# Performance work log

Hardware: AMD Instinct MI355X
Metric: run time of the kernel (lower is better)

## Reference

```python
import jax, jax.numpy as jnp
import numpy as np

B, C, H, W, K = 2, 36, 512, 512, 9
GROUPS, GSIZE = 3, 12  # channel groups 0:12, 12:24, 24:36


def _grid_sample_bilinear(feat, gx, gy):
    """Bilinear grid_sample, align_corners=True. feat [B,C,H,W]; gx,gy [B,H,W] in [-1,1]."""
    Bn, Cn, Hn, Wn = feat.shape
    px = (gx + 1.0) * 0.5 * (Wn - 1)
    py = (gy + 1.0) * 0.5 * (Hn - 1)
    x0 = jnp.floor(px)
    y0 = jnp.floor(py)
    wx = (px - x0)[:, None, :, :]
    wy = (py - y0)[:, None, :, :]
    x0i = jnp.clip(x0.astype(jnp.int32), 0, Wn - 1)
    x1i = jnp.clip(x0i + 1, 0, Wn - 1)
    y0i = jnp.clip(y0.astype(jnp.int32), 0, Hn - 1)
    y1i = jnpip = jnp.clip(y0.astype(jnp.int32) + 1, 0, Hn - 1)
    flat = feat.reshape(Bn, Cn, Hn * Wn)
    gather = jax.vmap(lambda f, yi, xi: f[:, yi * Wn + xi])  # -> [B,C,H,W]
    v00 = gather(flat, y0i, x0i)
    v01 = gather(flat, y0i, x1i)
    v10 = gather(flat, y1i, x0i)
    v11 = gather(flat, y1i, x1i)
    return (v00 * (1 - wx) * (1 - wy) + v01 * wx * (1 - wy)
            + v10 * (1 - wx) * wy + v11 * wx * wy)


def setup_inputs() -> dict:
    key = jax.random.key(0)
    k1, k2, k3 = jax.random.split(key, 3)
    features = jax.random.normal(k1, (B, C, H, W), jnp.float32)
    offset_x = jax.random.normal(k2, (B, K, H, W), jnp.float32) * 16.0
    offset_y = jax.random.normal(k3, (B, K, H, W), jnp.float32) * 16.0
    left_x = jnp.broadcast_to(jnp.arange(W, dtype=jnp.float32)[None, None, None, :], (B, 1, H, W))
    left_y = jnp.broadcast_to(jnp.arange(H, dtype=jnp.float32)[None, None, :, None], (B, 1, H, W))
    return {"features": features, "offset_x": offset_x, "offset_y": offset_y,
            "left_x": jnp.array(left_x), "left_y": jnp.array(left_y)}


def reference(features, offset_x, offset_y, left_x, left_y):
    Hn, Wn = features.shape[2], features.shape[3]
    # clamp candidate coords to image, then normalize to [-1,1]
    rx = jnp.clip(left_x + offset_x, 0.0, Wn - 1)
    ry = jnp.clip(left_y + offset_y, 0.0, Hn - 1)
    gx = (rx - (Wn - 1) / 2.0) / ((Wn - 1) / 2.0)  # [B,K,H,W]
    gy = (ry - (Hn - 1) / 2.0) / ((Hn - 1) / 2.0)

    def per_candidate(g):
        gxk, gyk = g  # each [B,H,W]
        a = _grid_sample_bilinear(features, gxk, gyk)  # [B,36,H,W]
        a2 = jnp.roll(a, 12, axis=1)
        a3 = jnp.roll(a, 24, axis=1)

        def grp_mean(d):  # [B,36,H,W] -> [B,3,H,W] mean over 12-channel groups
            return d.reshape(d.shape[0], GROUPS, GSIZE, d.shape[2], d.shape[3]).mean(axis=2)

        s = jnp.concatenate([grp_mean(-jnp.abs(features - a)),
                             grp_mean(-jnp.abs(features - a2)),
                             grp_mean(-jnp.abs(features - a3))], axis=1)  # [B,9,H,W]
        return jnp.max(s, axis=1)  # top-1 of sort == max  -> [B,H,W]

    strengths = jax.lax.map(per_candidate,
                            (jnp.moveaxis(gx, 1, 0), jnp.moveaxis(gy, 1, 0)))  # [K,B,H,W]
    strengths = jnp.moveaxis(strengths, 0, 1)  # [B,K,H,W]

    wgt = jax.nn.softmax(strengths * 1000.0, axis=1)
    ox = jnp.sum(offset_x * wgt, axis=1, keepdims=True)
    oy = jnp.sum(offset_y * wgt, axis=1, keepdims=True)
    oy = jnp.clip(oy + left_y, 0.0, Hn - 1) - left_y
    ox = jnp.clip(ox + left_x, 0.0, Wn - 1) - left_x
    return ox, oy
```

## Files before the change

kernel.cpp:

```cpp
#include <hip/hip_runtime.h>
#include <math.h>

#define B_ 2
#define C_ 36
#define H_ 512
#define W_ 512
#define K_ 9
#define HW_ (H_ * W_)
#define ROWF4 (W_ * C_ / 4)

__global__ __launch_bounds__(256) void transpose_kernel(const float* __restrict__ in,
                                                        float* __restrict__ out) {
  __shared__ float tile[64][37];
  int blk = blockIdx.x;
  int wt = blk & 7;
  int h = (blk >> 3) & (H_ - 1);
  int b = blk >> 12;
  int w0 = wt << 6;
  int tid = threadIdx.x;
  const float* src = in + ((size_t)b * C_) * HW_ + (size_t)h * W_ + w0;
#pragma unroll
  for (int it = 0; it < 9; ++it) {
    int idx = it * 256 + tid;
    int c = idx >> 6;
    int wl = idx & 63;
    tile[wl][c] = src[(size_t)c * HW_ + wl];
  }
  __syncthreads();
  float* dst = out + (((size_t)b * H_ + h) * W_ + w0) * C_;
#pragma unroll
  for (int it = 0; it < 9; ++it) {
    int idx = it * 256 + tid;
    int wl = idx / 36;
    int c = idx - wl * 36;
    dst[idx] = tile[wl][c];
  }
}

__global__ __launch_bounds__(64) void eval_kernel_cw(const float* __restrict__ feat,
                                                     const float* __restrict__ offx,
                                                     const float* __restrict__ offy,
                                                     float* __restrict__ out) {
  __shared__ __align__(16) float F_lds[64 * 36];
  __shared__ __align__(16) float4 w_lds[64];
  __shared__ int a_lds[64];
  __shared__ float xk_lds[64 * 9];

  int tid = threadIdx.x;
  int blk = blockIdx.x;
  int region = blk & 7;
  int slot = blk >> 3;
  int b = region >> 2;
  int qd = region & 3;
  int qy = (qd >> 1) << 8;
  int qx = (qd & 1) << 8;
  int tr = slot >> 5;
  int tc = slot & 31;
  if (tr & 1) tc = 31 - tc;
  int h = qy + tr * 8 + (tid >> 3);
  int w = qx + tc * 8 + (tid & 7);
  int ph = h * W_ + w;
  int p = b * HW_ + ph;

  const float4* feat4 = reinterpret_cast<const float4*>(feat);

  {
    const float4* myF = feat4 + (size_t)p * 9;
#pragma unroll
    for (int i = 0; i < 9; ++i) {
      float4 v = myF[i];
      *reinterpret_cast<float4*>(&F_lds[tid * 36 + 4 * i]) = v;
    }
  }

  int g = tid / 9;
  int q = tid - 9 * g;
  int qm3 = q % 3;
  int fofs = 4 * qm3;

  float lx = (float)w;
  float ly = (float)h;
  const float* oxb = offx + (size_t)b * K_ * HW_ + ph;
  const float* oyb = offy + (size_t)b * K_ * HW_ + ph;

  __syncthreads();

#pragma unroll 1
  for (int k = 0; k < K_; ++k) {
    float ox = oxb[k * HW_];
    float oy = oyb[k * HW_];
    float rx = fminf(fmaxf(lx + ox, 0.0f), 511.0f);
    float ry = fminf(fmaxf(ly + oy, 0.0f), 511.0f);
    float gx = (rx - 255.5f) / 255.5f;
    float gy = (ry - 255.5f) / 255.5f;
    float px = (gx + 1.0f) * 0.5f * 511.0f;
    float py = (gy + 1.0f) * 0.5f * 511.0f;
    int x0 = (int)floorf(px); x0 = (x0 > 510) ? 510 : x0;
    int y0 = (int)floorf(py); y0 = (y0 > 510) ? 510 : y0;
    float wx = px - (float)x0;
    float wy = py - (float)y0;
    float4 wv = make_float4((1.0f - wx) * (1.0f - wy), wx * (1.0f - wy),
                            (1.0f - wx) * wy, wx * wy);
    w_lds[tid] = wv;
    a_lds[tid] = ((b * H_ + y0) * W_ + x0) * 9;
    __syncthreads();

    for (int r = 0; r < 10; ++r) {
      int tt = 7 * r + g;
      int t = (tt > 63) ? 63 : tt;
      int tb = a_lds[t];
      float4 W4 = w_lds[t];
      const float4* r0 = feat4 + tb;
      float4 v00 = r0[q];
      float4 v01 = r0[9 + q];
      float4 v10 = r0[ROWF4 + q];
      float4 v11 = r0[ROWF4 + 9 + q];
      float4 a4;
      a4.x = W4.x * v00.x + W4.y * v01.x + W4.z * v10.x + W4.w * v11.x;
      a4.y = W4.x * v00.y + W4.y * v01.y + W4.z * v10.y + W4.w * v11.y;
      a4.z = W4.x * v00.z + W4.y * v01.z + W4.z * v10.z + W4.w * v11.z;
      a4.w = W4.x * v00.w + W4.y * v01.w + W4.z * v10.w + W4.w * v11.w;
      const float* fl = &F_lds[t * 36 + fofs];
      float4 f0 = *reinterpret_cast<const float4*>(fl);
      float4 f1 = *reinterpret_cast<const float4*>(fl + 12);
      float4 f2 = *reinterpret_cast<const float4*>(fl + 24);
      float pf0 = fabsf(f0.x - a4.x) + fabsf(f0.y - a4.y) +
                  fabsf(f0.z - a4.z) + fabsf(f0.w - a4.w);
      float pf1 = fabsf(f1.x - a4.x) + fabsf(f1.y - a4.y) +
                  fabsf(f1.z - a4.z) + fabsf(f1.w - a4.w);
      float pf2 = fabsf(f2.x - a4.x) + fabsf(f2.y - a4.y) +
                  fabsf(f2.z - a4.z) + fabsf(f2.w - a4.w);
      float d0 = pf0 + __shfl(pf0, tid + 1) + __shfl(pf0, tid + 2);
      float d1 = pf1 + __shfl(pf1, tid + 1) + __shfl(pf1, tid + 2);
      float d2 = pf2 + __shfl(pf2, tid + 1) + __shfl(pf2, tid + 2);
      float mn3 = fminf(d0, fminf(d1, d2));
      float mn = fminf(mn3, fminf(__shfl(mn3, tid + 3), __shfl(mn3, tid + 6)));
      if (q == 0 && g < 7 && tt < 64) {
        xk_lds[tt * 9 + k] = -(mn / 12.0f) * 1000.0f;
      }
    }
    __syncthreads();
  }

  float M = -INFINITY;
#pragma unroll
  for (int k = 0; k < K_; ++k) M = fmaxf(M, xk_lds[tid * 9 + k]);
  float den = 0.f, ax = 0.f, ay = 0.f;
#pragma unroll
  for (int k = 0; k < K_; ++k) {
    float e = expf(xk_lds[tid * 9 + k] - M);
    den += e;
    ax += e * oxb[k * HW_];
    ay += e * oyb[k * HW_];
  }
  float resx = ax / den;
  float resy = ay / den;
  out[p] = fminf(fmaxf(resx + lx, 0.0f), 511.0f) - lx;
  out[B_ * HW_ + p] = fminf(fmaxf(resy + ly, 0.0f), 511.0f) - ly;
}

__global__ __launch_bounds__(256) void eval_kernel_n(const float* __restrict__ feat,
                                                     const float* __restrict__ offx,
                                                     const float* __restrict__ offy,
                                                     float* __restrict__ out) {
  int p = blockIdx.x * 256 + threadIdx.x;
  int ph = p & (HW_ - 1);
  int b = p >> 18;
  float F[C_];
  const float* fb = feat + (size_t)b * C_ * HW_ + ph;
#pragma unroll
  for (int c = 0; c < C_; ++c) F[c] = fb[(size_t)c * HW_];
  float lx = (float)(ph & (W_ - 1));
  float ly = (float)((ph >> 9) & (H_ - 1));
  const float* oxb = offx + (size_t)b * K_ * HW_ + ph;
  const float* oyb = offy + (size_t)b * K_ * HW_ + ph;
  float M = -INFINITY, den = 0.f, ax = 0.f, ay = 0.f;
#pragma unroll 1
  for (int k = 0; k < K_; ++k) {
    float ox = oxb[k * HW_];
    float oy = oyb[k * HW_];
    float rx = fminf(fmaxf(lx + ox, 0.0f), 511.0f);
    float ry = fminf(fmaxf(ly + oy, 0.0f), 511.0f);
    float gx = (rx - 255.5f) / 255.5f;
    float gy = (ry - 255.5f) / 255.5f;
    float px = (gx + 1.0f) * 0.5f * 511.0f;
    float py = (gy + 1.0f) * 0.5f * 511.0f;
    int x0 = (int)floorf(px); x0 = (x0 > 510) ? 510 : x0;
    int y0 = (int)floorf(py); y0 = (y0 > 510) ? 510 : y0;
    float wx = px - (float)x0;
    float wy = py - (float)y0;
    float w00 = (1.0f - wx) * (1.0f - wy);
    float w01 = wx * (1.0f - wy);
    float w10 = (1.0f - wx) * wy;
    float w11 = wx * wy;
    float D[9] = {0.f, 0.f, 0.f, 0.f, 0.f, 0.f, 0.f, 0.f, 0.f};
    const float* pl = feat + (size_t)b * C_ * HW_ + (size_t)y0 * W_ + x0;
#pragma unroll
    for (int c = 0; c < C_; ++c) {
      const float* q0 = pl + (size_t)c * HW_;
      float v00 = q0[0], v01 = q0[1];
      float v10 = q0[W_], v11 = q0[W_ + 1];
      float a = v00 * w00 + v01 * w01 + v10 * w10 + v11 * w11;
      int i = c % 12;
      int ga = c / 12;
      D[ga]     += fabsf(F[i]      - a);
      D[3 + ga] += fabsf(F[12 + i] - a);
      D[6 + ga] += fabsf(F[24 + i] - a);
    }
    float mn = D[0];
#pragma unroll
    for (int j = 1; j < 9; ++j) mn = fminf(mn, D[j]);
    float xk = -(mn / 12.0f) * 1000.0f;
    float nm = fmaxf(M, xk);
    float sc = expf(M - nm);
    float ek = expf(xk - nm);
    den = den * sc + ek;
    ax = ax * sc + ox * ek;
    ay = ay * sc + oy * ek;
    M = nm;
  }
  float resx = ax / den;
  float resy = ay / den;
  out[p] = fminf(fmaxf(resx + lx, 0.0f), 511.0f) - lx;
  out[B_ * HW_ + p] = fminf(fmaxf(resy + ly, 0.0f), 511.0f) - ly;
}

extern "C" void kernel_launch(void* const* d_in, const int* in_sizes, int n_in,
                              void* d_out, int out_size, void* d_ws, size_t ws_size,
                              hipStream_t stream) {
  const float* features = (const float*)d_in[0];
  const float* offset_x = (const float*)d_in[1];
  const float* offset_y = (const float*)d_in[2];
  float* out = (float*)d_out;

  const int npix = B_ * HW_;
  const size_t need = (size_t)npix * C_ * sizeof(float);

  if (ws_size >= need) {
    float* featT = (float*)d_ws;
    transpose_kernel<<<B_ * H_ * (W_ / 64), 256, 0, stream>>>(features, featT);
    eval_kernel_cw<<<npix / 64, 64, 0, stream>>>(featT, offset_x, offset_y, out);
  } else {
    eval_kernel_n<<<npix / 256, 256, 0, stream>>>(features, offset_x, offset_y, out);
  }
}
```

Baseline: 349.1 us.

## Split bilinear gather from per-pixel distance reduction via LDS scratch

```diff
diff --git a/kernel.cpp b/kernel.cpp
--- a/kernel.cpp
+++ b/kernel.cpp
@@ -37,14 +37,13 @@
   }
 }
 
-__global__ __launch_bounds__(64) void eval_kernel_cw(const float* __restrict__ feat,
-                                                     const float* __restrict__ offx,
-                                                     const float* __restrict__ offy,
-                                                     float* __restrict__ out) {
-  __shared__ __align__(16) float F_lds[64 * 36];
+__global__ __launch_bounds__(64, 4) void eval_kernel_cw(const float* __restrict__ feat,
+                                                        const float* __restrict__ offx,
+                                                        const float* __restrict__ offy,
+                                                        float* __restrict__ out) {
+  __shared__ __align__(16) float scratch[64 * 36];
   __shared__ __align__(16) float4 w_lds[64];
   __shared__ int a_lds[64];
-  __shared__ float xk_lds[64 * 9];
 
   int tid = threadIdx.x;
   int blk = blockIdx.x;
@@ -64,26 +63,25 @@
 
   const float4* feat4 = reinterpret_cast<const float4*>(feat);
 
+  float F[C_];
   {
     const float4* myF = feat4 + (size_t)p * 9;
 #pragma unroll
     for (int i = 0; i < 9; ++i) {
       float4 v = myF[i];
-      *reinterpret_cast<float4*>(&F_lds[tid * 36 + 4 * i]) = v;
+      F[4 * i + 0] = v.x; F[4 * i + 1] = v.y; F[4 * i + 2] = v.z; F[4 * i + 3] = v.w;
     }
   }
 
   int g = tid / 9;
   int q = tid - 9 * g;
-  int qm3 = q % 3;
-  int fofs = 4 * qm3;
 
   float lx = (float)w;
   float ly = (float)h;
   const float* oxb = offx + (size_t)b * K_ * HW_ + ph;
   const float* oyb = offy + (size_t)b * K_ * HW_ + ph;
 
-  __syncthreads();
+  float M = -INFINITY, den = 0.f, axs = 0.f, ays = 0.f;
 
 #pragma unroll 1
   for (int k = 0; k < K_; ++k) {
@@ -99,14 +97,14 @@
     int y0 = (int)floorf(py); y0 = (y0 > 510) ? 510 : y0;
     float wx = px - (float)x0;
     float wy = py - (float)y0;
-    float4 wv = make_float4((1.0f - wx) * (1.0f - wy), wx * (1.0f - wy),
-                            (1.0f - wx) * wy, wx * wy);
-    w_lds[tid] = wv;
+    w_lds[tid] = make_float4((1.0f - wx) * (1.0f - wy), wx * (1.0f - wy),
+                             (1.0f - wx) * wy, wx * wy);
     a_lds[tid] = ((b * H_ + y0) * W_ + x0) * 9;
     __syncthreads();
 
+    int tt = g;
+#pragma unroll 1
     for (int r = 0; r < 10; ++r) {
-      int tt = 7 * r + g;
       int t = (tt > 63) ? 63 : tt;
       int tb = a_lds[t];
       float4 W4 = w_lds[t];
@@ -120,41 +118,44 @@
       a4.y = W4.x * v00.y + W4.y * v01.y + W4.z * v10.y + W4.w * v11.y;
       a4.z = W4.x * v00.z + W4.y * v01.z + W4.z * v10.z + W4.w * v11.z;
       a4.w = W4.x * v00.w + W4.y * v01.w + W4.z * v10.w + W4.w * v11.w;
-      const float* fl = &F_lds[t * 36 + fofs];
-      float4 f0 = *reinterpret_cast<const float4*>(fl);
-      float4 f1 = *reinterpret_cast<const float4*>(fl + 12);
-      float4 f2 = *reinterpret_cast<const float4*>(fl + 24);
-      float pf0 = fabsf(f0.x - a4.x) + fabsf(f0.y - a4.y) +
-                  fabsf(f0.z - a4.z) + fabsf(f0.w - a4.w);
-      float pf1 = fabsf(f1.x - a4.x) + fabsf(f1.y - a4.y) +
-                  fabsf(f1.z - a4.z) + fabsf(f1.w - a4.w);
-      float pf2 = fabsf(f2.x - a4.x) + fabsf(f2.y - a4.y) +
-                  fabsf(f2.z - a4.z) + fabsf(f2.w - a4.w);
-      float d0 = pf0 + __shfl(pf0, tid + 1) + __shfl(pf0, tid + 2);
-      float d1 = pf1 + __shfl(pf1, tid + 1) + __shfl(pf1, tid + 2);
-      float d2 = pf2 + __shfl(pf2, tid + 1) + __shfl(pf2, tid + 2);
-      float mn3 = fminf(d0, fminf(d1, d2));
-      float mn = fminf(mn3, fminf(__shfl(mn3, tid + 3), __shfl(mn3, tid + 6)));
-      if (q == 0 && g < 7 && tt < 64) {
-        xk_lds[tt * 9 + k] = -(mn / 12.0f) * 1000.0f;
+      if (tt < 64 && tid < 63) {
+        *reinterpret_cast<float4*>(&scratch[t * 36 + 4 * q]) = a4;
       }
+      tt += 7;
     }
     __syncthreads();
-  }
-
-  float M = -INFINITY;
-#pragma unroll
-  for (int k = 0; k < K_; ++k) M = fmaxf(M, xk_lds[tid * 9 + k]);
-  float den = 0.f, ax = 0.f, ay = 0.f;
-#pragma unroll
-  for (int k = 0; k < K_; ++k) {
-    float e = expf(xk_lds[tid * 9 + k] - M);
-    den += e;
-    ax += e * oxb[k * HW_];
-    ay += e * oyb[k * HW_];
-  }
-  float resx = ax / den;
-  float resy = ay / den;
+
+    float D[9] = {0.f, 0.f, 0.f, 0.f, 0.f, 0.f, 0.f, 0.f, 0.f};
+    const float4* sc = reinterpret_cast<const float4*>(&scratch[tid * 36]);
+#pragma unroll
+    for (int q2 = 0; q2 < 9; ++q2) {
+      float4 a4 = sc[q2];
+      float av[4] = {a4.x, a4.y, a4.z, a4.w};
+      int ga = q2 / 3;
+      int f0 = 4 * (q2 % 3);
+#pragma unroll
+      for (int j = 0; j < 4; ++j) {
+        D[ga]     += fabsf(F[f0 + j]      - av[j]);
+        D[3 + ga] += fabsf(F[12 + f0 + j] - av[j]);
+        D[6 + ga] += fabsf(F[24 + f0 + j] - av[j]);
+      }
+    }
+    float mn = D[0];
+#pragma unroll
+    for (int j = 1; j < 9; ++j) mn = fminf(mn, D[j]);
+    float xk = -(mn / 12.0f) * 1000.0f;
+
+    float nm = fmaxf(M, xk);
+    float scl = expf(M - nm);
+    float ek = expf(xk - nm);
+    den = den * scl + ek;
+    axs = axs * scl + ox * ek;
+    ays = ays * scl + oy * ek;
+    M = nm;
+  }
+
+  float resx = axs / den;
+  float resy = ays / den;
   out[p] = fminf(fmaxf(resx + lx, 0.0f), 511.0f) - lx;
   out[B_ * HW_ + p] = fminf(fmaxf(resy + ly, 0.0f), 511.0f) - ly;
 }
```

Measured after the change: 342.0 us. 2.0% less time.
